# Kernel tuning notes

Measured on AMD Instinct MI355X. Metric: run time of the kernel, lower is better.

The kernel has to match this reference:

```python
import jax, jax.numpy as jnp
import numpy as np

VOCAB = 50000
EMB = 512          # embedding_dim == hidden_size
E = 16             # num_experts
FFN = 2048         # deepspeed default expert FFN = 4*hidden
OUT = 2            # output_dim (sentiment classes)
B = 8192           # batch (tokens routed through MoE)
S = 64             # sequence length
CAP = B // E       # top-1 gate capacity, capacity_factor=1.0, min_capacity=0


def setup_inputs() -> dict:
    key = jax.random.key(0)
    ks = jax.random.split(key, 8)
    sc = lambda d: 1.0 / np.sqrt(d)
    return {
        "x": jax.random.randint(ks[0], (B, S), 0, VOCAB),
        "emb": jax.random.normal(ks[1], (VOCAB, EMB), jnp.float32) * 0.02,
        "wg": jax.random.normal(ks[2], (EMB, E), jnp.float32) * sc(EMB),
        "w1": jax.random.normal(ks[3], (E, EMB, FFN), jnp.float32) * sc(EMB),
        "b1": jnp.zeros((E, FFN), jnp.float32),
        "w2": jax.random.normal(ks[4], (E, FFN, EMB), jnp.float32) * sc(FFN),
        "b2": jnp.zeros((E, EMB), jnp.float32),
        "fc_w": jax.random.normal(ks[5], (EMB, OUT), jnp.float32) * sc(EMB),
        "fc_b": jnp.zeros((OUT,), jnp.float32),
    }


def _moe_top1(xm, wg, w1, b1, w2, b2):
    # deepspeed TopKGate(k=1): softmax gate, argmax expert, capacity drop
    gates = jax.nn.softmax(xm @ wg, axis=-1)                 # [B,E]
    idx = jnp.argmax(gates, axis=-1)                         # [B]
    mask1 = jax.nn.one_hot(idx, E, dtype=xm.dtype)           # [B,E]
    locs = jnp.cumsum(mask1, axis=0) - 1.0                   # slot within each expert
    mask1 = mask1 * (locs < CAP)                             # drop overflow tokens
    pos = jnp.sum(locs * mask1, axis=1).astype(jnp.int32)    # [B]
    gate_s = jnp.sum(gates * mask1, axis=1)                  # [B] gate of kept expert
    loc_oh = jax.nn.one_hot(pos, CAP, dtype=xm.dtype) * jnp.sum(mask1, axis=1, keepdims=True)
    combine = gate_s[:, None, None] * mask1[:, :, None] * loc_oh[:, None, :]  # [B,E,C]
    dispatch = (combine > 0).astype(xm.dtype)                # bool dispatch mask
    xe = jnp.einsum('bec,bm->ecm', dispatch, xm)             # [E,C,M] dispatched tokens
    h = jax.nn.relu(jnp.einsum('ecm,emf->ecf', xe, w1) + b1[:, None, :])
    ye = jnp.einsum('ecf,efm->ecm', h, w2) + b2[:, None, :]  # per-expert FFN
    return jnp.einsum('bec,ecm->bm', combine, ye)            # gate-weighted combine


def reference(x, emb, wg, w1, b1, w2, b2, fc_w, fc_b):
    xm = emb[x].mean(axis=1)                                 # [B,EMB] mean-pooled embeddings
    y = _moe_top1(xm, wg, w1, b1, w2, b2)                    # [B,EMB]
    return jax.nn.log_softmax(y @ fc_w + fc_b, axis=1)       # [B,OUT]
```

## Files before the change

kernel.cpp:

```cpp
#include <hip/hip_runtime.h>
#include <hip/hip_bf16.h>

#define NTOK 8192
#define SEQ 64
#define EMBD 512
#define NEXP 16
#define FFND 2048
#define CAPS 512

typedef __attribute__((ext_vector_type(8))) short short8;
typedef __attribute__((ext_vector_type(4))) float f32x4;

typedef const __attribute__((address_space(1))) unsigned int* as1_u32p;
typedef __attribute__((address_space(3))) unsigned int* as3_u32p;

__device__ __forceinline__ unsigned short f2bf(float f) {
  union { float f; unsigned u; } a; a.f = f;
  unsigned r = (a.u + 0x7fff + ((a.u >> 16) & 1)) >> 16;
  return (unsigned short)r;
}
__device__ __forceinline__ float bf2f(unsigned short h) {
  union { unsigned u; float f; } a; a.u = ((unsigned)h) << 16; return a.f;
}

__global__ void convert_emb(const float* __restrict__ in, unsigned short* __restrict__ out, int n8) {
  int i = blockIdx.x * blockDim.x + threadIdx.x;
  if (i >= n8) return;
  float4 v0 = ((const float4*)in)[i * 2];
  float4 v1 = ((const float4*)in)[i * 2 + 1];
  short8 o;
  o[0] = (short)f2bf(v0.x); o[1] = (short)f2bf(v0.y); o[2] = (short)f2bf(v0.z); o[3] = (short)f2bf(v0.w);
  o[4] = (short)f2bf(v1.x); o[5] = (short)f2bf(v1.y); o[6] = (short)f2bf(v1.z); o[7] = (short)f2bf(v1.w);
  ((short8*)out)[i] = o;
}

__global__ void transpose_bf16(const float* __restrict__ in, unsigned short* __restrict__ out,
                               int R, int C) {
  __shared__ float tile[32][33];
  int e = blockIdx.z;
  int c0 = blockIdx.x * 32, r0 = blockIdx.y * 32;
  const float* ip = in + (size_t)e * R * C;
  unsigned short* op = out + (size_t)e * R * C;
  int tx = threadIdx.x, ty = threadIdx.y;
  #pragma unroll
  for (int i = 0; i < 32; i += 8)
    tile[ty + i][tx] = ip[(size_t)(r0 + ty + i) * C + c0 + tx];
  __syncthreads();
  #pragma unroll
  for (int i = 0; i < 32; i += 8)
    op[(size_t)(c0 + ty + i) * R + r0 + tx] = f2bf(tile[tx][ty + i]);
}

__global__ void pool_gate_kernel(const int* __restrict__ x, const unsigned short* __restrict__ embb,
                                 const float* __restrict__ wg, unsigned short* __restrict__ xmb,
                                 int* __restrict__ eidx, float* __restrict__ gate) {
  int tok = blockIdx.x * 2 + (threadIdx.x >> 6);
  int lane = threadIdx.x & 63;
  int xi = x[tok * SEQ + lane];
  float a[8];
  #pragma unroll
  for (int j = 0; j < 8; j++) a[j] = 0.f;
  const short8* base = (const short8*)embb;
  #pragma unroll 8
  for (int s = 0; s < SEQ; s++) {
    int row = __shfl(xi, s);
    short8 v = base[(size_t)row * 64 + lane];
    #pragma unroll
    for (int j = 0; j < 8; j++) a[j] += bf2f((unsigned short)v[j]);
  }
  #pragma unroll
  for (int j = 0; j < 8; j++) a[j] *= (1.0f / 64.0f);
  short8 o;
  #pragma unroll
  for (int j = 0; j < 8; j++) o[j] = (short)f2bf(a[j]);
  *(short8*)(xmb + (size_t)tok * EMBD + lane * 8) = o;
  float p[16];
  #pragma unroll
  for (int e2 = 0; e2 < 16; e2++) p[e2] = 0.f;
  #pragma unroll
  for (int j = 0; j < 8; j++) {
    const float4* wr = (const float4*)(wg + (size_t)(lane * 8 + j) * NEXP);
    float4 q0 = wr[0], q1 = wr[1], q2 = wr[2], q3 = wr[3];
    p[0] += a[j] * q0.x; p[1] += a[j] * q0.y; p[2] += a[j] * q0.z; p[3] += a[j] * q0.w;
    p[4] += a[j] * q1.x; p[5] += a[j] * q1.y; p[6] += a[j] * q1.z; p[7] += a[j] * q1.w;
    p[8] += a[j] * q2.x; p[9] += a[j] * q2.y; p[10] += a[j] * q2.z; p[11] += a[j] * q2.w;
    p[12] += a[j] * q3.x; p[13] += a[j] * q3.y; p[14] += a[j] * q3.z; p[15] += a[j] * q3.w;
  }
  #pragma unroll
  for (int d = 1; d < 64; d <<= 1) {
    #pragma unroll
    for (int e2 = 0; e2 < 16; e2++) p[e2] += __shfl_xor(p[e2], d);
  }
  float best = p[0]; int bi = 0;
  #pragma unroll
  for (int e2 = 1; e2 < 16; e2++) { if (p[e2] > best) { best = p[e2]; bi = e2; } }
  float ssum = 0.f;
  #pragma unroll
  for (int e2 = 0; e2 < 16; e2++) ssum += __expf(p[e2] - best);
  if (lane == 0) { eidx[tok] = bi; gate[tok] = 1.0f / ssum; }
}

__global__ void assign_kernel(const int* __restrict__ eidx, int* __restrict__ slot,
                              int* __restrict__ dest) {
  __shared__ int sidx[NTOK];
  int tid = threadIdx.x;
  for (int i = tid; i < NTOK; i += 1024) { sidx[i] = eidx[i]; dest[i] = 0; }
  __syncthreads();
  int e = tid >> 6;
  int lane = tid & 63;
  int run = 0;
  for (int c = 0; c < NTOK; c += 64) {
    int v = sidx[c + lane];
    unsigned long long m = __ballot(v == e);
    int before = __popcll(m & ((1ull << lane) - 1ull));
    if (v == e) {
      int sl = run + before;
      if (sl < CAPS) { slot[c + lane] = sl; dest[e * CAPS + sl] = c + lane; }
      else slot[c + lane] = -1;
    }
    run += __popcll(m);
  }
}

template <int LDK, int NTOTL, int KSPLIT, bool GATHER, bool RELU_BF16>
__global__ __launch_bounds__(256) void gemm_moe(
    const unsigned short* __restrict__ A0, const int* __restrict__ dest,
    const unsigned short* __restrict__ BT, const float* __restrict__ bias,
    unsigned short* __restrict__ hout, float* __restrict__ yout) {
  __shared__ unsigned short Als[128 * 64];
  __shared__ unsigned short Bls[128 * 64];
  __shared__ int tokrow[128];

  const int e = blockIdx.z / KSPLIT;
  const int ksp = blockIdx.z % KSPLIT;
  const int kbase = ksp * (LDK / KSPLIT);
  const int n0 = blockIdx.x * 128;
  const int m0 = blockIdx.y * 128;
  const int tid = threadIdx.x;
  const int lane = tid & 63;
  const int wv = tid >> 6;
  const int wr = (wv >> 1) * 64;
  const int wc = (wv & 1) * 64;
  const int l15 = lane & 15;
  const int lhi = lane >> 4;

  if (GATHER) {
    if (tid < 128) tokrow[tid] = dest[e * CAPS + m0 + tid];
  }
  __syncthreads();

  const int r8 = lane >> 3, c8 = lane & 7;
  const char* asrc[4];
  const char* bsrc[4];
  char* adst[4];
  char* bdst[4];
  #pragma unroll
  for (int i = 0; i < 4; i++) {
    int row = i * 32 + wv * 8 + r8;
    int sw = (c8 * 16) ^ ((row & 7) << 4);
    size_t arow = GATHER ? (size_t)tokrow[row] : (size_t)(e * CAPS + m0 + row);
    asrc[i] = (const char*)(A0 + arow * LDK + kbase) + sw;
    bsrc[i] = (const char*)(BT + ((size_t)e * NTOTL + n0 + row) * LDK + kbase) + sw;
    adst[i] = (char*)Als + (size_t)(i * 32 + wv * 8) * 128;
    bdst[i] = (char*)Bls + (size_t)(i * 32 + wv * 8) * 128;
  }

  f32x4 acc[4][4];
  #pragma unroll
  for (int a = 0; a < 4; a++)
    #pragma unroll
    for (int b = 0; b < 4; b++) acc[a][b] = (f32x4){0.f, 0.f, 0.f, 0.f};

  const int NK = (LDK / KSPLIT) / 64;
  for (int kt = 0; kt < NK; kt++) {
    __syncthreads();
    #pragma unroll
    for (int i = 0; i < 4; i++) {
      __builtin_amdgcn_global_load_lds((as1_u32p)(const void*)(asrc[i] + kt * 128),
                                       (as3_u32p)(void*)adst[i], 16, 0, 0);
      __builtin_amdgcn_global_load_lds((as1_u32p)(const void*)(bsrc[i] + kt * 128),
                                       (as3_u32p)(void*)bdst[i], 16, 0, 0);
    }
    __syncthreads();
    #pragma unroll
    for (int ks = 0; ks < 2; ks++) {
      short8 af[4], bfr[4];
      #pragma unroll
      for (int mi = 0; mi < 4; mi++) {
        int row = wr + mi * 16 + l15;
        int off = row * 128 + (((ks * 32 + lhi * 8) * 2) ^ ((row & 7) << 4));
        af[mi] = *(const short8*)((const char*)Als + off);
      }
      #pragma unroll
      for (int ni = 0; ni < 4; ni++) {
        int row = wc + ni * 16 + l15;
        int off = row * 128 + (((ks * 32 + lhi * 8) * 2) ^ ((row & 7) << 4));
        bfr[ni] = *(const short8*)((const char*)Bls + off);
      }
      #pragma unroll
      for (int mi = 0; mi < 4; mi++)
        #pragma unroll
        for (int ni = 0; ni < 4; ni++)
          acc[mi][ni] = __builtin_amdgcn_mfma_f32_16x16x32_bf16(af[mi], bfr[ni], acc[mi][ni], 0, 0, 0);
    }
  }

  float* yp = yout + (size_t)ksp * ((size_t)NEXP * CAPS * NTOTL);
  #pragma unroll
  for (int ni = 0; ni < 4; ni++) {
    int col = n0 + wc + ni * 16 + l15;
    float bs = RELU_BF16 ? bias[e * NTOTL + col] : 0.f;
    #pragma unroll
    for (int mi = 0; mi < 4; mi++) {
      f32x4 v = acc[mi][ni];
      #pragma unroll
      for (int j = 0; j < 4; j++) {
        int row = m0 + wr + mi * 16 + lhi * 4 + j;
        float xv = v[j] + bs;
        size_t oidx = ((size_t)(e * CAPS + row)) * NTOTL + col;
        if (RELU_BF16) hout[oidx] = f2bf(fmaxf(xv, 0.f));
        else           yp[oidx] = xv;
      }
    }
  }
}

__global__ void combine_kernel(const float* __restrict__ ye0, const float* __restrict__ ye1,
                               const float* __restrict__ b2, const int* __restrict__ eidx,
                               const int* __restrict__ slot, const float* __restrict__ gate,
                               const float* __restrict__ fcw, const float* __restrict__ fcb,
                               float* __restrict__ out) {
  int b = blockIdx.x * 4 + (threadIdx.x >> 6);
  int lane = threadIdx.x & 63;
  int s = slot[b];
  float z0, z1;
  if (s >= 0) {
    int e = eidx[b];
    size_t off = ((size_t)(e * CAPS + s)) * EMBD;
    float a0 = 0, a1 = 0;
    #pragma unroll
    for (int i = 0; i < EMBD / 64; i++) {
      int c = lane + i * 64;
      float v = ye0[off + c] + ye1[off + c] + b2[e * EMBD + c];
      a0 += v * fcw[c * 2 + 0];
      a1 += v * fcw[c * 2 + 1];
    }
    #pragma unroll
    for (int d = 1; d < 64; d <<= 1) { a0 += __shfl_xor(a0, d); a1 += __shfl_xor(a1, d); }
    float g = gate[b];
    z0 = g * a0 + fcb[0];
    z1 = g * a1 + fcb[1];
  } else {
    z0 = fcb[0]; z1 = fcb[1];
  }
  if (lane == 0) {
    float m = fmaxf(z0, z1);
    float lse = m + logf(expf(z0 - m) + expf(z1 - m));
    out[(size_t)b * 2 + 0] = z0 - lse;
    out[(size_t)b * 2 + 1] = z1 - lse;
  }
}

extern "C" void kernel_launch(void* const* d_in, const int* in_sizes, int n_in,
                              void* d_out, int out_size, void* d_ws, size_t ws_size,
                              hipStream_t stream) {
  const int* x = (const int*)d_in[0];
  const float* emb = (const float*)d_in[1];
  const float* wg = (const float*)d_in[2];
  const float* w1 = (const float*)d_in[3];
  const float* b1 = (const float*)d_in[4];
  const float* w2 = (const float*)d_in[5];
  const float* b2 = (const float*)d_in[6];
  const float* fcw = (const float*)d_in[7];
  const float* fcb = (const float*)d_in[8];
  float* out = (float*)d_out;

  char* ws = (char*)d_ws;
  unsigned short* w2T = (unsigned short*)(ws + 0);
  unsigned short* w1T = (unsigned short*)(ws + 33554432);
  float* ye0          = (float*)(ws + 33554432);
  float* ye1          = ye0 + (size_t)NEXP * CAPS * EMBD;
  unsigned short* embb= (unsigned short*)(ws + 67108864);
  unsigned short* h   = (unsigned short*)(ws + 67108864);
  unsigned short* xmb = (unsigned short*)(ws + 118308864);
  int* eidx           = (int*)(ws + 126697472);
  float* gate         = (float*)(ws + 126730240);
  int* slot           = (int*)(ws + 126763008);
  int* dest           = (int*)(ws + 126795776);

  convert_emb<<<12500, 256, 0, stream>>>(emb, embb, (50000 * EMBD) / 8);
  transpose_bf16<<<dim3(FFND / 32, EMBD / 32, NEXP), dim3(32, 8), 0, stream>>>(w1, w1T, EMBD, FFND);
  transpose_bf16<<<dim3(EMBD / 32, FFND / 32, NEXP), dim3(32, 8), 0, stream>>>(w2, w2T, FFND, EMBD);
  pool_gate_kernel<<<NTOK / 2, 128, 0, stream>>>(x, embb, wg, xmb, eidx, gate);
  assign_kernel<<<1, 1024, 0, stream>>>(eidx, slot, dest);
  gemm_moe<EMBD, FFND, 1, true, true><<<dim3(FFND / 128, CAPS / 128, NEXP), 256, 0, stream>>>(
      xmb, dest, w1T, b1, h, nullptr);
  gemm_moe<FFND, EMBD, 2, false, false><<<dim3(EMBD / 128, CAPS / 128, NEXP * 2), 256, 0, stream>>>(
      h, nullptr, w2T, nullptr, nullptr, ye0);
  combine_kernel<<<NTOK / 4, 256, 0, stream>>>(ye0, ye1, b2, eidx, slot, gate, fcw, fcb, out);
}
```

Before: 460.6 us.

## Fuse weight/embedding preprocessing, split pooling across waves, store expert outputs in bf16

Merges the embedding bf16 conversion and both weight transposes into one launch, and widens the transpose tiles to 64x64 with vectorized float4 reads and short8 writes. Pooling now runs one token per 256-thread block, with four waves each preloading 16 rows before an LDS reduction. The split-K second GEMM writes its partial sums in bf16 instead of fp32, and the combine step reads them vectorized. This cuts launch count and memory traffic, at the cost of some precision in the partial sums and lower per-wave work in pooling.

```diff
diff --git a/kernel.cpp b/kernel.cpp
--- a/kernel.cpp
+++ b/kernel.cpp
@@ -7,6 +7,7 @@
 #define NEXP 16
 #define FFND 2048
 #define CAPS 512
+#define VOCABSZ 3200000
 
 typedef __attribute__((ext_vector_type(8))) short short8;
 typedef __attribute__((ext_vector_type(4))) float f32x4;
@@ -23,57 +24,97 @@
   union { unsigned u; float f; } a; a.u = ((unsigned)h) << 16; return a.f;
 }
 
-__global__ void convert_emb(const float* __restrict__ in, unsigned short* __restrict__ out, int n8) {
-  int i = blockIdx.x * blockDim.x + threadIdx.x;
-  if (i >= n8) return;
-  float4 v0 = ((const float4*)in)[i * 2];
-  float4 v1 = ((const float4*)in)[i * 2 + 1];
-  short8 o;
-  o[0] = (short)f2bf(v0.x); o[1] = (short)f2bf(v0.y); o[2] = (short)f2bf(v0.z); o[3] = (short)f2bf(v0.w);
-  o[4] = (short)f2bf(v1.x); o[5] = (short)f2bf(v1.y); o[6] = (short)f2bf(v1.z); o[7] = (short)f2bf(v1.w);
-  ((short8*)out)[i] = o;
-}
-
-__global__ void transpose_bf16(const float* __restrict__ in, unsigned short* __restrict__ out,
-                               int R, int C) {
-  __shared__ float tile[32][33];
-  int e = blockIdx.z;
-  int c0 = blockIdx.x * 32, r0 = blockIdx.y * 32;
-  const float* ip = in + (size_t)e * R * C;
-  unsigned short* op = out + (size_t)e * R * C;
-  int tx = threadIdx.x, ty = threadIdx.y;
-  #pragma unroll
-  for (int i = 0; i < 32; i += 8)
-    tile[ty + i][tx] = ip[(size_t)(r0 + ty + i) * C + c0 + tx];
-  __syncthreads();
-  #pragma unroll
-  for (int i = 0; i < 32; i += 8)
-    op[(size_t)(c0 + ty + i) * R + r0 + tx] = f2bf(tile[tx][ty + i]);
-}
-
-__global__ void pool_gate_kernel(const int* __restrict__ x, const unsigned short* __restrict__ embb,
-                                 const float* __restrict__ wg, unsigned short* __restrict__ xmb,
-                                 int* __restrict__ eidx, float* __restrict__ gate) {
-  int tok = blockIdx.x * 2 + (threadIdx.x >> 6);
-  int lane = threadIdx.x & 63;
-  int xi = x[tok * SEQ + lane];
+__global__ __launch_bounds__(256) void preprocess_kernel(
+    const float* __restrict__ emb, const float* __restrict__ w1, const float* __restrict__ w2,
+    unsigned short* __restrict__ embb, unsigned short* __restrict__ w1T,
+    unsigned short* __restrict__ w2T) {
+  const int z = blockIdx.z;
+  const int tid = threadIdx.x;
+  if (z >= 32) {
+    const int n8 = VOCABSZ;
+    int i = ((z - 32) * 256 + (int)(blockIdx.y * 32 + blockIdx.x)) * 256 + tid;
+    if (i < n8) {
+      float4 v0 = ((const float4*)emb)[i * 2];
+      float4 v1 = ((const float4*)emb)[i * 2 + 1];
+      short8 o;
+      o[0] = (short)f2bf(v0.x); o[1] = (short)f2bf(v0.y); o[2] = (short)f2bf(v0.z); o[3] = (short)f2bf(v0.w);
+      o[4] = (short)f2bf(v1.x); o[5] = (short)f2bf(v1.y); o[6] = (short)f2bf(v1.z); o[7] = (short)f2bf(v1.w);
+      ((short8*)embb)[i] = o;
+    }
+    return;
+  }
+  __shared__ float tile[64][65];
+  const float* ip; unsigned short* op; int R, C, r0, c0;
+  if (z < 16) {
+    R = EMBD; C = FFND;
+    ip = w1 + (size_t)z * R * C; op = w1T + (size_t)z * R * C;
+    c0 = blockIdx.x * 64; r0 = blockIdx.y * 64;
+  } else {
+    R = FFND; C = EMBD;
+    ip = w2 + (size_t)(z - 16) * R * C; op = w2T + (size_t)(z - 16) * R * C;
+    r0 = blockIdx.x * 64; c0 = blockIdx.y * 64;
+  }
+  #pragma unroll
+  for (int p = 0; p < 4; p++) {
+    int r = p * 16 + (tid >> 4), cg = (tid & 15) * 4;
+    float4 v = *(const float4*)(ip + (size_t)(r0 + r) * C + c0 + cg);
+    tile[r][cg + 0] = v.x; tile[r][cg + 1] = v.y; tile[r][cg + 2] = v.z; tile[r][cg + 3] = v.w;
+  }
+  __syncthreads();
+  #pragma unroll
+  for (int q = 0; q < 2; q++) {
+    int c = q * 32 + (tid >> 3), rch = (tid & 7) * 8;
+    short8 o;
+    #pragma unroll
+    for (int i = 0; i < 8; i++) o[i] = (short)f2bf(tile[rch + i][c]);
+    *(short8*)(op + (size_t)(c0 + c) * R + r0 + rch) = o;
+  }
+}
+
+__global__ __launch_bounds__(256) void pool_gate_kernel(
+    const int* __restrict__ x, const unsigned short* __restrict__ embb,
+    const float* __restrict__ wg, unsigned short* __restrict__ xmb,
+    int* __restrict__ eidx, float* __restrict__ gate) {
+  __shared__ float part[4][EMBD];
+  __shared__ float xs[EMBD];
+  const int tok = blockIdx.x;
+  const int tid = threadIdx.x;
+  const int w = tid >> 6, lane = tid & 63;
+  int xi = 0;
+  if (lane < 16) xi = x[tok * SEQ + w * 16 + lane];
+  const short8* base = (const short8*)embb;
+  short8 vv[16];
+  #pragma unroll
+  for (int s = 0; s < 16; s++) {
+    int row = __shfl(xi, s);
+    vv[s] = base[(size_t)row * 64 + lane];
+  }
   float a[8];
   #pragma unroll
   for (int j = 0; j < 8; j++) a[j] = 0.f;
-  const short8* base = (const short8*)embb;
-  #pragma unroll 8
-  for (int s = 0; s < SEQ; s++) {
-    int row = __shfl(xi, s);
-    short8 v = base[(size_t)row * 64 + lane];
-    #pragma unroll
-    for (int j = 0; j < 8; j++) a[j] += bf2f((unsigned short)v[j]);
-  }
-  #pragma unroll
-  for (int j = 0; j < 8; j++) a[j] *= (1.0f / 64.0f);
-  short8 o;
-  #pragma unroll
-  for (int j = 0; j < 8; j++) o[j] = (short)f2bf(a[j]);
-  *(short8*)(xmb + (size_t)tok * EMBD + lane * 8) = o;
+  #pragma unroll
+  for (int s = 0; s < 16; s++)
+    #pragma unroll
+    for (int j = 0; j < 8; j++) a[j] += bf2f((unsigned short)vv[s][j]);
+  *(f32x4*)&part[w][lane * 8]     = (f32x4){a[0], a[1], a[2], a[3]};
+  *(f32x4*)&part[w][lane * 8 + 4] = (f32x4){a[4], a[5], a[6], a[7]};
+  __syncthreads();
+  {
+    int c = tid * 2;
+    float s0 = (part[0][c] + part[1][c] + part[2][c] + part[3][c]) * (1.f / 64.f);
+    float s1 = (part[0][c + 1] + part[1][c + 1] + part[2][c + 1] + part[3][c + 1]) * (1.f / 64.f);
+    xs[c] = s0; xs[c + 1] = s1;
+    ((unsigned*)xmb)[tok * 256 + tid] = ((unsigned)f2bf(s1) << 16) | f2bf(s0);
+  }
+  __syncthreads();
+  if (w != 0) return;
+  float g[8];
+  {
+    float4 v0 = *(const float4*)&xs[lane * 8];
+    float4 v1 = *(const float4*)&xs[lane * 8 + 4];
+    g[0] = v0.x; g[1] = v0.y; g[2] = v0.z; g[3] = v0.w;
+    g[4] = v1.x; g[5] = v1.y; g[6] = v1.z; g[7] = v1.w;
+  }
   float p[16];
   #pragma unroll
   for (int e2 = 0; e2 < 16; e2++) p[e2] = 0.f;
@@ -81,10 +122,10 @@
   for (int j = 0; j < 8; j++) {
     const float4* wr = (const float4*)(wg + (size_t)(lane * 8 + j) * NEXP);
     float4 q0 = wr[0], q1 = wr[1], q2 = wr[2], q3 = wr[3];
-    p[0] += a[j] * q0.x; p[1] += a[j] * q0.y; p[2] += a[j] * q0.z; p[3] += a[j] * q0.w;
-    p[4] += a[j] * q1.x; p[5] += a[j] * q1.y; p[6] += a[j] * q1.z; p[7] += a[j] * q1.w;
-    p[8] += a[j] * q2.x; p[9] += a[j] * q2.y; p[10] += a[j] * q2.z; p[11] += a[j] * q2.w;
-    p[12] += a[j] * q3.x; p[13] += a[j] * q3.y; p[14] += a[j] * q3.z; p[15] += a[j] * q3.w;
+    p[0] += g[j] * q0.x; p[1] += g[j] * q0.y; p[2]  += g[j] * q0.z; p[3]  += g[j] * q0.w;
+    p[4] += g[j] * q1.x; p[5] += g[j] * q1.y; p[6]  += g[j] * q1.z; p[7]  += g[j] * q1.w;
+    p[8] += g[j] * q2.x; p[9] += g[j] * q2.y; p[10] += g[j] * q2.z; p[11] += g[j] * q2.w;
+    p[12] += g[j] * q3.x; p[13] += g[j] * q3.y; p[14] += g[j] * q3.z; p[15] += g[j] * q3.w;
   }
   #pragma unroll
   for (int d = 1; d < 64; d <<= 1) {
@@ -122,11 +163,11 @@
   }
 }
 
-template <int LDK, int NTOTL, int KSPLIT, bool GATHER, bool RELU_BF16>
+template <int LDK, int NTOTL, int KSPLIT, bool GATHER, bool RELU_BIAS>
 __global__ __launch_bounds__(256) void gemm_moe(
     const unsigned short* __restrict__ A0, const int* __restrict__ dest,
     const unsigned short* __restrict__ BT, const float* __restrict__ bias,
-    unsigned short* __restrict__ hout, float* __restrict__ yout) {
+    unsigned short* __restrict__ hout) {
   __shared__ unsigned short Als[128 * 64];
   __shared__ unsigned short Bls[128 * 64];
   __shared__ int tokrow[128];
@@ -205,11 +246,11 @@
     }
   }
 
-  float* yp = yout + (size_t)ksp * ((size_t)NEXP * CAPS * NTOTL);
+  unsigned short* hp = hout + (size_t)ksp * ((size_t)NEXP * CAPS * NTOTL);
   #pragma unroll
   for (int ni = 0; ni < 4; ni++) {
     int col = n0 + wc + ni * 16 + l15;
-    float bs = RELU_BF16 ? bias[e * NTOTL + col] : 0.f;
+    float bs = RELU_BIAS ? bias[e * NTOTL + col] : 0.f;
     #pragma unroll
     for (int mi = 0; mi < 4; mi++) {
       f32x4 v = acc[mi][ni];
@@ -218,14 +259,14 @@
         int row = m0 + wr + mi * 16 + lhi * 4 + j;
         float xv = v[j] + bs;
         size_t oidx = ((size_t)(e * CAPS + row)) * NTOTL + col;
-        if (RELU_BF16) hout[oidx] = f2bf(fmaxf(xv, 0.f));
-        else           yp[oidx] = xv;
+        hp[oidx] = f2bf(RELU_BIAS ? fmaxf(xv, 0.f) : xv);
       }
     }
   }
 }
 
-__global__ void combine_kernel(const float* __restrict__ ye0, const float* __restrict__ ye1,
+__global__ void combine_kernel(const unsigned short* __restrict__ ye0,
+                               const unsigned short* __restrict__ ye1,
                                const float* __restrict__ b2, const int* __restrict__ eidx,
                                const int* __restrict__ slot, const float* __restrict__ gate,
                                const float* __restrict__ fcw, const float* __restrict__ fcb,
@@ -236,14 +277,21 @@
   float z0, z1;
   if (s >= 0) {
     int e = eidx[b];
-    size_t off = ((size_t)(e * CAPS + s)) * EMBD;
+    size_t off = ((size_t)(e * CAPS + s)) * EMBD + lane * 8;
+    short8 v0 = *(const short8*)(ye0 + off);
+    short8 v1 = *(const short8*)(ye1 + off);
+    const float4* bb = (const float4*)(b2 + e * EMBD + lane * 8);
+    float4 b20 = bb[0], b21 = bb[1];
+    float bv[8] = {b20.x, b20.y, b20.z, b20.w, b21.x, b21.y, b21.z, b21.w};
+    const float4* fw = (const float4*)(fcw + lane * 16);
     float a0 = 0, a1 = 0;
     #pragma unroll
-    for (int i = 0; i < EMBD / 64; i++) {
-      int c = lane + i * 64;
-      float v = ye0[off + c] + ye1[off + c] + b2[e * EMBD + c];
-      a0 += v * fcw[c * 2 + 0];
-      a1 += v * fcw[c * 2 + 1];
+    for (int j = 0; j < 8; j++) {
+      float v = bf2f((unsigned short)v0[j]) + bf2f((unsigned short)v1[j]) + bv[j];
+      float4 q = fw[j >> 1];
+      float w0 = (j & 1) ? q.z : q.x;
+      float w1 = (j & 1) ? q.w : q.y;
+      a0 += v * w0; a1 += v * w1;
     }
     #pragma unroll
     for (int d = 1; d < 64; d <<= 1) { a0 += __shfl_xor(a0, d); a1 += __shfl_xor(a1, d); }
@@ -278,24 +326,22 @@
   char* ws = (char*)d_ws;
   unsigned short* w2T = (unsigned short*)(ws + 0);
   unsigned short* w1T = (unsigned short*)(ws + 33554432);
-  float* ye0          = (float*)(ws + 33554432);
-  float* ye1          = ye0 + (size_t)NEXP * CAPS * EMBD;
+  unsigned short* ye0 = (unsigned short*)(ws + 33554432);
+  unsigned short* ye1 = ye0 + (size_t)NEXP * CAPS * EMBD;
   unsigned short* embb= (unsigned short*)(ws + 67108864);
   unsigned short* h   = (unsigned short*)(ws + 67108864);
-  unsigned short* xmb = (unsigned short*)(ws + 118308864);
-  int* eidx           = (int*)(ws + 126697472);
-  float* gate         = (float*)(ws + 126730240);
-  int* slot           = (int*)(ws + 126763008);
-  int* dest           = (int*)(ws + 126795776);
-
-  convert_emb<<<12500, 256, 0, stream>>>(emb, embb, (50000 * EMBD) / 8);
-  transpose_bf16<<<dim3(FFND / 32, EMBD / 32, NEXP), dim3(32, 8), 0, stream>>>(w1, w1T, EMBD, FFND);
-  transpose_bf16<<<dim3(EMBD / 32, FFND / 32, NEXP), dim3(32, 8), 0, stream>>>(w2, w2T, FFND, EMBD);
-  pool_gate_kernel<<<NTOK / 2, 128, 0, stream>>>(x, embb, wg, xmb, eidx, gate);
+  unsigned short* xmb = (unsigned short*)(ws + 121634816);
+  int* eidx           = (int*)(ws + 130023424);
+  float* gate         = (float*)(ws + 130056192);
+  int* slot           = (int*)(ws + 130088960);
+  int* dest           = (int*)(ws + 130121728);
+
+  preprocess_kernel<<<dim3(32, 8, 96), 256, 0, stream>>>(emb, w1, w2, embb, w1T, w2T);
+  pool_gate_kernel<<<NTOK, 256, 0, stream>>>(x, embb, wg, xmb, eidx, gate);
   assign_kernel<<<1, 1024, 0, stream>>>(eidx, slot, dest);
   gemm_moe<EMBD, FFND, 1, true, true><<<dim3(FFND / 128, CAPS / 128, NEXP), 256, 0, stream>>>(
-      xmb, dest, w1T, b1, h, nullptr);
+      xmb, dest, w1T, b1, h);
   gemm_moe<FFND, EMBD, 2, false, false><<<dim3(EMBD / 128, CAPS / 128, NEXP * 2), 256, 0, stream>>>(
-      h, nullptr, w2T, nullptr, nullptr, ye0);
+      h, nullptr, w2T, nullptr, ye0);
   combine_kernel<<<NTOK / 4, 256, 0, stream>>>(ye0, ye1, b2, eidx, slot, gate, fcw, fcb, out);
 }
```

Result: faster. 427.2 us (-7.3%).
